# Performance work log

Measured on AMD Instinct MI355X. Metric: run time of the kernel, lower is better.

Reference implementation:

```python
import jax, jax.numpy as jnp
import numpy as np

NUM_NODES = 50000
NUM_EDGES = 800000
IN_CH = 128
OUT_CH = 128


def setup_inputs() -> dict:
    key = jax.random.key(0)
    k1, k2, k3, k4 = jax.random.split(key, 4)
    x = jax.random.normal(k1, (NUM_NODES, IN_CH), dtype=jnp.float32)
    edge_index = jax.random.randint(k2, (2, NUM_EDGES), 0, NUM_NODES, dtype=jnp.int64)
    # nn.Linear params (W: [out, in], b: [out]) with torch-like init scale
    scale = 1.0 / np.sqrt(IN_CH)
    W = jax.random.uniform(k3, (OUT_CH, IN_CH), dtype=jnp.float32, minval=-scale, maxval=scale)
    b = jax.random.uniform(k4, (OUT_CH,), dtype=jnp.float32, minval=-scale, maxval=scale)
    return {"x": x, "edge_index": edge_index, "W": W, "b": b}


def reference(x, edge_index, W, b):
    # x: [N, Cin], edge_index: [2, E]
    x_t = x @ W.T + b  # [N, Cout]
    row, col = edge_index[0], edge_index[1]
    # sparse adj (row, col, 1.0) @ x_t == scatter-add of x_t[col] into row
    messages = x_t[col]  # [E, Cout]
    out = jax.ops.segment_sum(messages, row, num_segments=NUM_NODES)  # [N, Cout]
    return jnp.tanh(out)
```

## Files before the change

kernel.cpp:

```cpp
#include <hip/hip_runtime.h>
#include <hip/hip_bf16.h>
#include <hip/hip_fp16.h>
#include <math.h>

#define N_NODES 50000
#define N_EDGES 800000
#define CH 128

__global__ __launch_bounds__(256) void gemm_xt_f16(const float* __restrict__ x,
                                                   const float* __restrict__ W,
                                                   const float* __restrict__ bias_p,
                                                   __half* __restrict__ xt,
                                                   int rows_per_block) {
    __shared__ float wt[128 * 128];
    __shared__ float xs[32][128];

    const int tid = threadIdx.x;
    const int cg  = tid & 31;
    const int rg  = tid >> 5;

    for (int i = tid; i < 128 * 128; i += 256) {
        int c = i >> 7, k = i & 127;
        wt[(k << 7) + ((((c >> 2) ^ (k & 31))) << 2) + (c & 3)] = W[i];
    }
    const float4 bias = reinterpret_cast<const float4*>(bias_p)[cg];
    __syncthreads();

    const int row0    = blockIdx.x * rows_per_block;
    const int row_end = min(row0 + rows_per_block, N_NODES);

    for (int rb = row0; rb < row_end; rb += 32) {
        #pragma unroll
        for (int p = 0; p < 4; ++p) {
            const int r    = p * 8 + rg;
            const int grow = rb + r;
            float4 f = {0.f, 0.f, 0.f, 0.f};
            if (grow < N_NODES)
                f = reinterpret_cast<const float4*>(&x[(size_t)grow * CH])[cg];
            reinterpret_cast<float4*>(&xs[r][0])[cg] = f;
        }
        __syncthreads();

        float acc[4][4];
        #pragma unroll
        for (int i = 0; i < 4; ++i)
            #pragma unroll
            for (int j = 0; j < 4; ++j) acc[i][j] = 0.f;

        const int r0 = 4 * rg;
        #pragma unroll 8
        for (int k = 0; k < 128; ++k) {
            const float4 wv = *reinterpret_cast<const float4*>(
                &wt[(k << 7) + ((cg ^ (k & 31)) << 2)]);
            const float x0 = xs[r0 + 0][k];
            const float x1 = xs[r0 + 1][k];
            const float x2 = xs[r0 + 2][k];
            const float x3 = xs[r0 + 3][k];
            acc[0][0] += x0 * wv.x; acc[0][1] += x0 * wv.y;
            acc[0][2] += x0 * wv.z; acc[0][3] += x0 * wv.w;
            acc[1][0] += x1 * wv.x; acc[1][1] += x1 * wv.y;
            acc[1][2] += x1 * wv.z; acc[1][3] += x1 * wv.w;
            acc[2][0] += x2 * wv.x; acc[2][1] += x2 * wv.y;
            acc[2][2] += x2 * wv.z; acc[2][3] += x2 * wv.w;
            acc[3][0] += x3 * wv.x; acc[3][1] += x3 * wv.y;
            acc[3][2] += x3 * wv.z; acc[3][3] += x3 * wv.w;
        }

        #pragma unroll
        for (int i = 0; i < 4; ++i) {
            const int grow = rb + r0 + i;
            if (grow < N_NODES) {
                float2 lo = make_float2(acc[i][0] + bias.x, acc[i][1] + bias.y);
                float2 hi = make_float2(acc[i][2] + bias.z, acc[i][3] + bias.w);
                __half2 h01 = __float22half2_rn(lo);
                __half2 h23 = __float22half2_rn(hi);
                uint2 pk;
                pk.x = *reinterpret_cast<unsigned int*>(&h01);
                pk.y = *reinterpret_cast<unsigned int*>(&h23);
                *reinterpret_cast<uint2*>(&xt[(size_t)grow * CH + 4 * cg]) = pk;
            }
        }
        __syncthreads();
    }
}

__global__ __launch_bounds__(256) void build_ll(const int* __restrict__ ei,
                                                int* __restrict__ head,
                                                int2* __restrict__ ll) {
    const int e = blockIdx.x * 256 + threadIdx.x;
    if (e < N_EDGES) {
        const int row = ei[e];
        const int col = ei[N_EDGES + e];
        const int h   = (e & 3) * N_NODES + row;
        const int old = atomicExch(&head[h], e);
        ll[e] = make_int2(old, col);
    }
}

__global__ __launch_bounds__(256) void gather_tanh(const int* __restrict__ head,
                                                   const int2* __restrict__ ll,
                                                   const __half* __restrict__ xt,
                                                   float* __restrict__ out) {
    const int node = (blockIdx.x * 256 + threadIdx.x) >> 6;
    if (node >= N_NODES) return;
    const int lane = threadIdx.x & 63;

    int e0 = head[node];
    int e1 = head[node + N_NODES];
    int e2 = head[node + 2 * N_NODES];
    int e3 = head[node + 3 * N_NODES];

    float ax = 0.f, ay = 0.f;
    while (e0 >= 0 || e1 >= 0 || e2 >= 0 || e3 >= 0) {
        int n0 = -1, c0 = -1, n1 = -1, c1 = -1;
        int n2 = -1, c2 = -1, n3 = -1, c3 = -1;
        if (e0 >= 0) { const int2 t = ll[e0]; n0 = t.x; c0 = t.y; }
        if (e1 >= 0) { const int2 t = ll[e1]; n1 = t.x; c1 = t.y; }
        if (e2 >= 0) { const int2 t = ll[e2]; n2 = t.x; c2 = t.y; }
        if (e3 >= 0) { const int2 t = ll[e3]; n3 = t.x; c3 = t.y; }
        if (c0 >= 0) {
            const float2 v = __half22float2(*reinterpret_cast<const __half2*>(
                &xt[(size_t)c0 * CH + lane * 2]));
            ax += v.x; ay += v.y;
        }
        if (c1 >= 0) {
            const float2 v = __half22float2(*reinterpret_cast<const __half2*>(
                &xt[(size_t)c1 * CH + lane * 2]));
            ax += v.x; ay += v.y;
        }
        if (c2 >= 0) {
            const float2 v = __half22float2(*reinterpret_cast<const __half2*>(
                &xt[(size_t)c2 * CH + lane * 2]));
            ax += v.x; ay += v.y;
        }
        if (c3 >= 0) {
            const float2 v = __half22float2(*reinterpret_cast<const __half2*>(
                &xt[(size_t)c3 * CH + lane * 2]));
            ax += v.x; ay += v.y;
        }
        e0 = n0; e1 = n1; e2 = n2; e3 = n3;
    }

    float2 o;
    o.x = tanhf(ax);
    o.y = tanhf(ay);
    *reinterpret_cast<float2*>(&out[(size_t)node * CH + lane * 2]) = o;
}

__global__ __launch_bounds__(256) void scatter_add(const int* __restrict__ ei,
                                                   const __half* __restrict__ xt,
                                                   float* __restrict__ out) {
    const int gid = blockIdx.x * 256 + threadIdx.x;
    const int e = gid >> 5;
    if (e >= N_EDGES) return;
    const int lane = gid & 31;
    const int row = ei[e];
    const int col = ei[N_EDGES + e];
    const float2 va = __half22float2(*reinterpret_cast<const __half2*>(
        &xt[(size_t)col * CH + lane * 4]));
    const float2 vb = __half22float2(*reinterpret_cast<const __half2*>(
        &xt[(size_t)col * CH + lane * 4 + 2]));
    float* dst = &out[(size_t)row * CH + lane * 4];
    atomicAdd(dst + 0, va.x);
    atomicAdd(dst + 1, va.y);
    atomicAdd(dst + 2, vb.x);
    atomicAdd(dst + 3, vb.y);
}

__global__ __launch_bounds__(256) void tanh_inplace(float* __restrict__ out) {
    const int i = blockIdx.x * 256 + threadIdx.x;
    if (i < N_NODES * CH / 4) {
        float4* p = reinterpret_cast<float4*>(out);
        float4 v = p[i];
        v.x = tanhf(v.x); v.y = tanhf(v.y);
        v.z = tanhf(v.z); v.w = tanhf(v.w);
        p[i] = v;
    }
}

extern "C" void kernel_launch(void* const* d_in, const int* in_sizes, int n_in,
                              void* d_out, int out_size, void* d_ws, size_t ws_size,
                              hipStream_t stream) {
    const float* x  = (const float*)d_in[0];
    const int*   ei = (const int*)d_in[1];
    const float* W  = (const float*)d_in[2];
    const float* b  = (const float*)d_in[3];
    float* out = (float*)d_out;

    const size_t XT_B    = (size_t)N_NODES * CH * sizeof(__half);
    const size_t HEAD_O  = XT_B;
    size_t LL_O = HEAD_O + (size_t)(4 * N_NODES) * 4;
    LL_O = (LL_O + 255) & ~(size_t)255;
    const size_t NEED = LL_O + (size_t)N_EDGES * 8;

    __half* xt = (__half*)d_ws;

    const int rpb = 96;
    const int gblocks = (N_NODES + rpb - 1) / rpb;
    gemm_xt_f16<<<gblocks, 256, 0, stream>>>(x, W, b, xt, rpb);

    if (ws_size >= NEED) {
        int*  head = (int*)((char*)d_ws + HEAD_O);
        int2* ll   = (int2*)((char*)d_ws + LL_O);

        hipMemsetAsync(head, 0xFF, (size_t)(4 * N_NODES) * 4, stream);
        const int eblocks = (N_EDGES + 255) / 256;
        build_ll<<<eblocks, 256, 0, stream>>>(ei, head, ll);

        const int nblocks = (N_NODES * 64 + 255) / 256;
        gather_tanh<<<nblocks, 256, 0, stream>>>(head, ll, xt, out);
    } else {
        hipMemsetAsync(d_out, 0, (size_t)N_NODES * CH * sizeof(float), stream);
        const int sblocks = (N_EDGES * 32 + 255) / 256;
        scatter_add<<<sblocks, 256, 0, stream>>>(ei, xt, out);
        const int tblocks = (N_NODES * CH / 4 + 255) / 256;
        tanh_inplace<<<tblocks, 256, 0, stream>>>(out);
    }
}
```

Baseline: 230.3 us.

## Replace FP32 SIMT GEMM with split-bf16 MFMA GEMM for linear transform

Rewrites the node-feature linear layer to use bf16 MFMA 16x16x32 instructions. Inputs and weights are split into high and low bf16 parts, and three MFMAs per tile approximate FP32 accuracy. Results are staged through LDS so the fp16 output is written with coalesced 16-byte stores. Each block now handles 64 rows and rebuilds the bf16 weight copies in LDS, which adds per-block conversion overhead and LDS use in exchange for much cheaper matrix math.

```diff
diff --git a/kernel.cpp b/kernel.cpp
--- a/kernel.cpp
+++ b/kernel.cpp
@@ -7,80 +7,109 @@
 #define N_EDGES 800000
 #define CH 128
 
-__global__ __launch_bounds__(256) void gemm_xt_f16(const float* __restrict__ x,
-                                                   const float* __restrict__ W,
-                                                   const float* __restrict__ bias_p,
-                                                   __half* __restrict__ xt,
-                                                   int rows_per_block) {
-    __shared__ float wt[128 * 128];
-    __shared__ float xs[32][128];
-
-    const int tid = threadIdx.x;
-    const int cg  = tid & 31;
-    const int rg  = tid >> 5;
-
-    for (int i = tid; i < 128 * 128; i += 256) {
-        int c = i >> 7, k = i & 127;
-        wt[(k << 7) + ((((c >> 2) ^ (k & 31))) << 2) + (c & 3)] = W[i];
-    }
-    const float4 bias = reinterpret_cast<const float4*>(bias_p)[cg];
+typedef __attribute__((ext_vector_type(8))) short bf16x8;
+typedef __attribute__((ext_vector_type(4))) float f32x4;
+
+static __device__ __forceinline__ short f2bf(float f) {
+    unsigned u = __builtin_bit_cast(unsigned, f);
+    unsigned r = (u + 0x7FFFu + ((u >> 16) & 1u)) >> 16;
+    return (short)r;
+}
+static __device__ __forceinline__ float bf2f(short s) {
+    unsigned u = ((unsigned)(unsigned short)s) << 16;
+    return __builtin_bit_cast(float, u);
+}
+
+__global__ __launch_bounds__(256) void gemm_xt_mfma(const float* __restrict__ x,
+                                                    const float* __restrict__ W,
+                                                    const float* __restrict__ bias_p,
+                                                    __half* __restrict__ xt) {
+    __shared__ short  whi[2048 * 8];
+    __shared__ short  wlo[2048 * 8];
+    __shared__ float  bias_lds[128];
+    __shared__ __half ostage[4][16 * 128];
+
+    const int tid  = threadIdx.x;
+    const int w    = tid >> 6;
+    const int lane = tid & 63;
+    const int rb   = blockIdx.x * 64;
+
+    #pragma unroll
+    for (int i = 0; i < 8; ++i) {
+        const int id   = tid + (i << 8);
+        const int ln   = id & 63;
+        const int ctkt = id >> 6;
+        const int c    = ((ctkt >> 2) << 4) + (ln & 15);
+        const int k0   = ((ctkt & 3) << 5) + ((ln >> 4) << 3);
+        const float4 f0 = *reinterpret_cast<const float4*>(&W[c * 128 + k0]);
+        const float4 f1 = *reinterpret_cast<const float4*>(&W[c * 128 + k0 + 4]);
+        bf16x8 vh, vl;
+        const float ff[8] = {f0.x, f0.y, f0.z, f0.w, f1.x, f1.y, f1.z, f1.w};
+        #pragma unroll
+        for (int j = 0; j < 8; ++j) {
+            const short h = f2bf(ff[j]);
+            vh[j] = h;
+            vl[j] = f2bf(ff[j] - bf2f(h));
+        }
+        reinterpret_cast<bf16x8*>(whi)[id] = vh;
+        reinterpret_cast<bf16x8*>(wlo)[id] = vl;
+    }
+    if (tid < 128) bias_lds[tid] = bias_p[tid];
     __syncthreads();
 
-    const int row0    = blockIdx.x * rows_per_block;
-    const int row_end = min(row0 + rows_per_block, N_NODES);
-
-    for (int rb = row0; rb < row_end; rb += 32) {
+    f32x4 acc[8];
+    #pragma unroll
+    for (int ct = 0; ct < 8; ++ct) acc[ct] = (f32x4){0.f, 0.f, 0.f, 0.f};
+
+    const int arow = rb + (w << 4) + (lane & 15);
+    #pragma unroll
+    for (int kt = 0; kt < 4; ++kt) {
+        const int k0 = (kt << 5) + ((lane >> 4) << 3);
+        bf16x8 ah = {0, 0, 0, 0, 0, 0, 0, 0};
+        bf16x8 al = {0, 0, 0, 0, 0, 0, 0, 0};
+        if (arow < N_NODES) {
+            const float4 f0 = *reinterpret_cast<const float4*>(&x[(size_t)arow * CH + k0]);
+            const float4 f1 = *reinterpret_cast<const float4*>(&x[(size_t)arow * CH + k0 + 4]);
+            const float ff[8] = {f0.x, f0.y, f0.z, f0.w, f1.x, f1.y, f1.z, f1.w};
+            #pragma unroll
+            for (int j = 0; j < 8; ++j) {
+                const short h = f2bf(ff[j]);
+                ah[j] = h;
+                al[j] = f2bf(ff[j] - bf2f(h));
+            }
+        }
         #pragma unroll
-        for (int p = 0; p < 4; ++p) {
-            const int r    = p * 8 + rg;
-            const int grow = rb + r;
-            float4 f = {0.f, 0.f, 0.f, 0.f};
-            if (grow < N_NODES)
-                f = reinterpret_cast<const float4*>(&x[(size_t)grow * CH])[cg];
-            reinterpret_cast<float4*>(&xs[r][0])[cg] = f;
-        }
-        __syncthreads();
-
-        float acc[4][4];
+        for (int ct = 0; ct < 8; ++ct) {
+            const int id = ((ct << 2) + kt) * 64 + lane;
+            const bf16x8 bh = reinterpret_cast<bf16x8*>(whi)[id];
+            const bf16x8 bl = reinterpret_cast<bf16x8*>(wlo)[id];
+            acc[ct] = __builtin_amdgcn_mfma_f32_16x16x32_bf16(ah, bh, acc[ct], 0, 0, 0);
+            acc[ct] = __builtin_amdgcn_mfma_f32_16x16x32_bf16(ah, bl, acc[ct], 0, 0, 0);
+            acc[ct] = __builtin_amdgcn_mfma_f32_16x16x32_bf16(al, bh, acc[ct], 0, 0, 0);
+        }
+    }
+
+    #pragma unroll
+    for (int ct = 0; ct < 8; ++ct) {
+        const int c  = (ct << 4) + (lane & 15);
+        const float bv = bias_lds[c];
         #pragma unroll
-        for (int i = 0; i < 4; ++i)
-            #pragma unroll
-            for (int j = 0; j < 4; ++j) acc[i][j] = 0.f;
-
-        const int r0 = 4 * rg;
-        #pragma unroll 8
-        for (int k = 0; k < 128; ++k) {
-            const float4 wv = *reinterpret_cast<const float4*>(
-                &wt[(k << 7) + ((cg ^ (k & 31)) << 2)]);
-            const float x0 = xs[r0 + 0][k];
-            const float x1 = xs[r0 + 1][k];
-            const float x2 = xs[r0 + 2][k];
-            const float x3 = xs[r0 + 3][k];
-            acc[0][0] += x0 * wv.x; acc[0][1] += x0 * wv.y;
-            acc[0][2] += x0 * wv.z; acc[0][3] += x0 * wv.w;
-            acc[1][0] += x1 * wv.x; acc[1][1] += x1 * wv.y;
-            acc[1][2] += x1 * wv.z; acc[1][3] += x1 * wv.w;
-            acc[2][0] += x2 * wv.x; acc[2][1] += x2 * wv.y;
-            acc[2][2] += x2 * wv.z; acc[2][3] += x2 * wv.w;
-            acc[3][0] += x3 * wv.x; acc[3][1] += x3 * wv.y;
-            acc[3][2] += x3 * wv.z; acc[3][3] += x3 * wv.w;
-        }
-
-        #pragma unroll
-        for (int i = 0; i < 4; ++i) {
-            const int grow = rb + r0 + i;
-            if (grow < N_NODES) {
-                float2 lo = make_float2(acc[i][0] + bias.x, acc[i][1] + bias.y);
-                float2 hi = make_float2(acc[i][2] + bias.z, acc[i][3] + bias.w);
-                __half2 h01 = __float22half2_rn(lo);
-                __half2 h23 = __float22half2_rn(hi);
-                uint2 pk;
-                pk.x = *reinterpret_cast<unsigned int*>(&h01);
-                pk.y = *reinterpret_cast<unsigned int*>(&h23);
-                *reinterpret_cast<uint2*>(&xt[(size_t)grow * CH + 4 * cg]) = pk;
-            }
-        }
-        __syncthreads();
+        for (int j = 0; j < 4; ++j) {
+            const int r_in = ((lane >> 4) << 2) + j;
+            ostage[w][r_in * 128 + c] = __float2half(acc[ct][j] + bv);
+        }
+    }
+    __syncthreads();
+
+    #pragma unroll
+    for (int j = 0; j < 4; ++j) {
+        const int cid  = (j << 6) + lane;
+        const int r_in = cid >> 4;
+        const int c0   = (cid & 15) << 3;
+        const int grow = rb + (w << 4) + r_in;
+        if (grow < N_NODES)
+            *reinterpret_cast<uint4*>(&xt[(size_t)grow * CH + c0]) =
+                *reinterpret_cast<const uint4*>(&ostage[w][r_in * 128 + c0]);
     }
 }
 
@@ -195,9 +224,8 @@
 
     __half* xt = (__half*)d_ws;
 
-    const int rpb = 96;
-    const int gblocks = (N_NODES + rpb - 1) / rpb;
-    gemm_xt_f16<<<gblocks, 256, 0, stream>>>(x, W, b, xt, rpb);
+    const int gblocks = (N_NODES + 63) / 64;
+    gemm_xt_mfma<<<gblocks, 256, 0, stream>>>(x, W, b, xt);
 
     if (ws_size >= NEED) {
         int*  head = (int*)((char*)d_ws + HEAD_O);
```

Result: faster. 211.8 us (-8.0%).
